# Kernel tuning notes

Hardware: AMD Instinct MI355X
Metric: run time of the kernel (lower is better)

The kernel has to match this reference:

```python
import jax, jax.numpy as jnp
import numpy as np

C = 128; D_STATE = 16; D_CONV = 4; EXPAND = 2
DI = EXPAND * C          # 256 inner dim
DT_RANK = (C + 15) // 16 # 8
NM, T, V = 32, 64, 22


def _mamba(x, in_w, conv_w, conv_b, xproj_w, dt_w, dt_b, Alog, Dp, out_w):
    """Standard Mamba block. x: (B, L, C) -> (B, L, C)."""
    B_, L, _ = x.shape
    xz = x @ in_w.T                       # (B, L, 2*DI)
    xi, z = jnp.split(xz, 2, axis=-1)     # each (B, L, DI)
    # causal depthwise conv over L, kernel D_CONV
    K = conv_w.shape[-1]
    xp = jnp.pad(xi, ((0, 0), (K - 1, 0), (0, 0)))
    xc = conv_b + sum(xp[:, k:k + L, :] * conv_w[:, k] for k in range(K))
    xc = jax.nn.silu(xc)
    dbl = xc @ xproj_w.T                  # (B, L, DT_RANK + 2*D_STATE)
    dt, Bm, Cm = jnp.split(dbl, [DT_RANK, DT_RANK + D_STATE], axis=-1)
    dt = jax.nn.softplus(dt @ dt_w.T + dt_b)   # (B, L, DI)
    A = -jnp.exp(Alog)                    # (DI, D_STATE), strictly negative

    def step(h, inp):
        dt_l, B_l, C_l, u_l = inp         # (B,DI) (B,DS) (B,DS) (B,DI)
        dA = jnp.exp(dt_l[:, :, None] * A)             # (B, DI, DS)
        h = dA * h + (dt_l * u_l)[:, :, None] * B_l[:, None, :]
        y = jnp.einsum('bds,bs->bd', h, C_l)
        return h, y

    h0 = jnp.zeros((B_, DI, D_STATE), x.dtype)
    xs = (jnp.moveaxis(dt, 1, 0), jnp.moveaxis(Bm, 1, 0),
          jnp.moveaxis(Cm, 1, 0), jnp.moveaxis(xc, 1, 0))
    _, ys = jax.lax.scan(step, h0, xs)    # ys: (L, B, DI)
    y = jnp.moveaxis(ys, 0, 1) + xc * Dp  # skip connection
    y = y * jax.nn.silu(z)
    return y @ out_w.T                    # (B, L, C)


def setup_inputs() -> dict:
    key = jax.random.key(0)
    ks = jax.random.split(key, 40)
    i = [0]
    def nrm(shape, s=0.05):
        i[0] += 1
        return jax.random.normal(ks[i[0]], shape, jnp.float32) * s
    inp = {"x": jax.random.normal(ks[0], (NM, C, T, V), jnp.float32)}
    for p in ("f", "b"):
        inp[p + "_in_w"] = nrm((2 * DI, C))
        inp[p + "_conv_w"] = nrm((DI, D_CONV), 0.2)
        inp[p + "_conv_b"] = nrm((DI,))
        inp[p + "_xproj_w"] = nrm((DT_RANK + 2 * D_STATE, DI))
        inp[p + "_dt_w"] = nrm((DI, DT_RANK), 0.1)
        inp[p + "_dt_b"] = nrm((DI,), 0.1)
        i[0] += 1
        inp[p + "_Alog"] = jax.random.uniform(ks[i[0]], (DI, D_STATE), jnp.float32)
        inp[p + "_D"] = nrm((DI,), 1.0)
        inp[p + "_out_w"] = nrm((C, DI))
    inp["fuse_w"] = nrm((C, 2 * C))
    inp["ln_w"] = jnp.ones((C,), jnp.float32)
    inp["ln_b"] = jnp.zeros((C,), jnp.float32)
    return inp


def reference(x, f_in_w, f_conv_w, f_conv_b, f_xproj_w, f_dt_w, f_dt_b, f_Alog, f_D, f_out_w,
              b_in_w, b_conv_w, b_conv_b, b_xproj_w, b_dt_w, b_dt_b, b_Alog, b_D, b_out_w,
              fuse_w, ln_w, ln_b):
    nm, c, t, v = x.shape
    xs = jnp.transpose(x, (0, 2, 3, 1)).reshape(nm * t, v, c)   # (B, V, C)
    fwd = _mamba(xs, f_in_w, f_conv_w, f_conv_b, f_xproj_w, f_dt_w, f_dt_b, f_Alog, f_D, f_out_w)
    bwd = _mamba(xs[:, ::-1, :], b_in_w, b_conv_w, b_conv_b, b_xproj_w, b_dt_w, b_dt_b, b_Alog, b_D, b_out_w)[:, ::-1, :]
    y = jnp.concatenate([fwd, bwd], axis=-1) @ fuse_w.T         # (B, V, C)
    mu = y.mean(-1, keepdims=True)
    var = y.var(-1, keepdims=True)
    y = (y - mu) / jnp.sqrt(var + 1e-5) * ln_w + ln_b
    return jnp.transpose(y.reshape(nm, t, v, c), (0, 3, 1, 2))  # (NM, C, T, V)
```

## Files before the change

kernel.cpp:

```cpp
#include <hip/hip_runtime.h>
#include <hip/hip_bf16.h>
#include <math.h>

namespace {

typedef unsigned short u16;
typedef unsigned int u32;

constexpr int LSEQ = 22, CD = 128, DI = 256, TDIM = 64;

constexpr int XS_LD = 136;
constexpr int XI_LD = 264;
constexpr int Y2_LD = 132;

constexpr int K1_XS = 0;
constexpr int K1_XI = 2992;
constexpr int K1_Z  = 8800;
constexpr int K1_N  = 14608;

constexpr int K2_N  = 11616;

constexpr int WS_F_IN_HI = 0;
constexpr int WS_F_IN_LO = 65536;
constexpr int WS_B_IN_HI = 131072;
constexpr int WS_B_IN_LO = 196608;
constexpr int WS_F_OUT   = 262144;
constexpr int WS_B_OUT   = 294912;
constexpr int WS_FUSE    = 327680;
constexpr int WS_F_XP_HI = 360448;
constexpr int WS_F_XP_LO = 372736;
constexpr int WS_B_XP_HI = 385024;
constexpr int WS_B_XP_LO = 397312;
constexpr int WS_TOTAL   = 409600;
constexpr int WS_Y       = 409600;

typedef __attribute__((ext_vector_type(8))) short bf16x8;
typedef __attribute__((ext_vector_type(4))) float f32x4;

__device__ __forceinline__ u16 f2bf(float f) {
  __bf16 b = (__bf16)f;
  return *reinterpret_cast<u16*>(&b);
}
__device__ __forceinline__ float bf2f(u16 h) {
  return __uint_as_float(((u32)h) << 16);
}
__device__ __forceinline__ float sigm(float x) {
  float e = __builtin_amdgcn_exp2f(-1.44269504f * x);
  return __builtin_amdgcn_rcpf(1.0f + e);
}

__global__ void prep_weights(const float* __restrict__ f_in, const float* __restrict__ b_in,
                             const float* __restrict__ f_xp, const float* __restrict__ b_xp,
                             u16* __restrict__ ws) {
  int i = blockIdx.x * 256 + threadIdx.x;
  if (i >= WS_TOTAL) return;
  u16 r = 0;
  if (i < WS_F_IN_LO) {
    r = f2bf(f_in[i]);
  } else if (i < WS_B_IN_HI) {
    float v = f_in[i - WS_F_IN_LO];
    r = f2bf(v - bf2f(f2bf(v)));
  } else if (i < WS_B_IN_LO) {
    r = f2bf(b_in[i - WS_B_IN_HI]);
  } else if (i < WS_F_OUT) {
    float v = b_in[i - WS_B_IN_LO];
    r = f2bf(v - bf2f(f2bf(v)));
  } else if (i < WS_F_XP_HI) {
    r = 0;
  } else if (i < WS_F_XP_LO) {
    int j = i - WS_F_XP_HI, n = j >> 8, k = j & 255;
    r = (n < 40) ? f2bf(f_xp[n * 256 + k]) : (u16)0;
  } else if (i < WS_B_XP_HI) {
    int j = i - WS_F_XP_LO, n = j >> 8, k = j & 255;
    if (n < 40) { float v = f_xp[n * 256 + k]; r = f2bf(v - bf2f(f2bf(v))); } else r = 0;
  } else if (i < WS_B_XP_LO) {
    int j = i - WS_B_XP_HI, n = j >> 8, k = j & 255;
    r = (n < 40) ? f2bf(b_xp[n * 256 + k]) : (u16)0;
  } else {
    int j = i - WS_B_XP_LO, n = j >> 8, k = j & 255;
    if (n < 40) { float v = b_xp[n * 256 + k]; r = f2bf(v - bf2f(f2bf(v))); } else r = 0;
  }
  ws[i] = r;
}

__global__ void prep_fold(const float* __restrict__ f_out, const float* __restrict__ b_out,
                          const float* __restrict__ fuse, u16* __restrict__ ws) {
  int i = blockIdx.x * 256 + threadIdx.x;
  int half = i >> 15;
  int j = i & 32767;
  int c = j >> 8, d = j & 255;
  const float* ow = half ? b_out : f_out;
  const float* fw = fuse + c * 256 + half * 128;
  float acc = 0.f;
#pragma unroll 4
  for (int k = 0; k < 128; ++k) acc = fmaf(fw[k], ow[k * 256 + d], acc);
  ws[(half ? WS_B_OUT : WS_F_OUT) + c * 256 + d] = f2bf(acc);
}

__global__ __launch_bounds__(256, 4) void mamba_scan_kernel(
    const float* __restrict__ x,
    const float* __restrict__ f_conv_w, const float* __restrict__ f_conv_b,
    const float* __restrict__ f_dt_w, const float* __restrict__ f_dt_b,
    const float* __restrict__ f_Alog, const float* __restrict__ f_D,
    const float* __restrict__ b_conv_w, const float* __restrict__ b_conv_b,
    const float* __restrict__ b_dt_w, const float* __restrict__ b_dt_b,
    const float* __restrict__ b_Alog, const float* __restrict__ b_D,
    u16* __restrict__ ws)
{
  __shared__ __align__(16) u16 pool[K1_N];

  u16* xs  = pool + K1_XS;
  u16* xiD = pool + K1_XI;
  u16* zD  = pool + K1_Z;

  const int tid = threadIdx.x;
  const int wv = tid >> 6, ln = tid & 63, lr = ln & 15, lg = ln >> 4;
  const int bid = blockIdx.x;
  const int b = bid >> 1, dir = bid & 1;
  const int nm = b / TDIM, t = b - nm * TDIM;
  const size_t base = (size_t)nm * CD * (TDIM * LSEQ) + (size_t)t * LSEQ;

  const int ra0 = (lr < LSEQ) ? lr : (LSEQ - 1);
  const int ra1 = (16 + lr < LSEQ) ? (16 + lr) : (LSEQ - 1);

#pragma unroll
  for (int k = 0; k < 11; ++k) {
    int idx = tid + k * 256;
    int c = idx / LSEQ, v = idx - c * LSEQ;
    xs[v * XS_LD + c] = f2bf(x[base + (size_t)c * (TDIM * LSEQ) + v]);
  }
  __syncthreads();

  {
    bf16x8 afr[2][4];
#pragma unroll
    for (int kt = 0; kt < 4; ++kt) {
      afr[0][kt] = *(const bf16x8*)&xs[ra0 * XS_LD + kt * 32 + lg * 8];
      afr[1][kt] = *(const bf16x8*)&xs[ra1 * XS_LD + kt * 32 + lg * 8];
    }
    const u16* ih = ws + (dir ? WS_B_IN_HI : WS_F_IN_HI);
    const u16* il = ws + (dir ? WS_B_IN_LO : WS_F_IN_LO);
    u16* dst = (wv < 2) ? xiD : zD;
    const bool isz = (wv >= 2);
    const int cb0 = (wv & 1) * 128;
#pragma unroll
    for (int half = 0; half < 2; ++half) {
      f32x4 acc[2][4];
#pragma unroll
      for (int m = 0; m < 2; ++m)
#pragma unroll
        for (int n = 0; n < 4; ++n) acc[m][n] = f32x4{0.f, 0.f, 0.f, 0.f};
#pragma unroll
      for (int kt = 0; kt < 4; ++kt) {
        bf16x8 bh[4], bl[4];
#pragma unroll
        for (int n = 0; n < 4; ++n) {
          const int off = (wv * 128 + (half * 4 + n) * 16 + lr) * 128 + kt * 32 + lg * 8;
          bh[n] = *(const bf16x8*)(ih + off);
          bl[n] = *(const bf16x8*)(il + off);
        }
#pragma unroll
        for (int n = 0; n < 4; ++n) {
          acc[0][n] = __builtin_amdgcn_mfma_f32_16x16x32_bf16(afr[0][kt], bh[n], acc[0][n], 0, 0, 0);
          acc[0][n] = __builtin_amdgcn_mfma_f32_16x16x32_bf16(afr[0][kt], bl[n], acc[0][n], 0, 0, 0);
          acc[1][n] = __builtin_amdgcn_mfma_f32_16x16x32_bf16(afr[1][kt], bh[n], acc[1][n], 0, 0, 0);
          acc[1][n] = __builtin_amdgcn_mfma_f32_16x16x32_bf16(afr[1][kt], bl[n], acc[1][n], 0, 0, 0);
        }
      }
#pragma unroll
      for (int m = 0; m < 2; ++m)
#pragma unroll
        for (int n = 0; n < 4; ++n)
#pragma unroll
          for (int j = 0; j < 4; ++j) {
            int row = 16 * m + lg * 4 + j;
            if (row < LSEQ) {
              int rr = dir ? (LSEQ - 1 - row) : row;
              float v = acc[m][n][j];
              if (isz) v = v * sigm(v);
              dst[rr * XI_LD + cb0 + half * 64 + n * 16 + lr] = f2bf(v);
            }
          }
    }
  }
  __syncthreads();

  {
    const int d = tid;
    const float* cw  = dir ? b_conv_w : f_conv_w;
    const float* cbp = dir ? b_conv_b : f_conv_b;
    float4 w4 = *(const float4*)(cw + d * 4);
    float bb = cbp[d];
    float w0 = 0.f, w1 = 0.f, w2 = 0.f;
    float nxt = bf2f(xiD[d]);
#pragma unroll
    for (int l = 0; l < LSEQ; ++l) {
      float w3 = nxt;
      if (l + 1 < LSEQ) nxt = bf2f(xiD[(l + 1) * XI_LD + d]);
      float a = fmaf(w0, w4.x, bb);
      a = fmaf(w1, w4.y, a);
      a = fmaf(w2, w4.z, a);
      a = fmaf(w3, w4.w, a);
      float s = a * sigm(a);
      xiD[l * XI_LD + d] = f2bf(s);
      w0 = w1; w1 = w2; w2 = w3;
    }
  }
  __syncthreads();

  for (int tt = wv; tt < 6; tt += 4) {
    const int mt = tt / 3, nt = tt - mt * 3;
    const u16* xph = ws + (dir ? WS_B_XP_HI : WS_F_XP_HI);
    const u16* xpl = ws + (dir ? WS_B_XP_LO : WS_F_XP_LO);
    const int raa = (mt * 16 + lr < LSEQ) ? (mt * 16 + lr) : (LSEQ - 1);
    f32x4 acc = f32x4{0.f, 0.f, 0.f, 0.f};
    const u16* bh_p = xph + (nt * 16 + lr) * 256 + lg * 8;
    const u16* bl_p = xpl + (nt * 16 + lr) * 256 + lg * 8;
#pragma unroll
    for (int kt = 0; kt < 8; kt += 2) {
      bf16x8 a0  = *(const bf16x8*)&xiD[raa * XI_LD + kt * 32 + lg * 8];
      bf16x8 a1  = *(const bf16x8*)&xiD[raa * XI_LD + (kt + 1) * 32 + lg * 8];
      bf16x8 bh0 = *(const bf16x8*)(bh_p + kt * 32);
      bf16x8 bl0 = *(const bf16x8*)(bl_p + kt * 32);
      bf16x8 bh1 = *(const bf16x8*)(bh_p + (kt + 1) * 32);
      bf16x8 bl1 = *(const bf16x8*)(bl_p + (kt + 1) * 32);
      acc = __builtin_amdgcn_mfma_f32_16x16x32_bf16(a0, bh0, acc, 0, 0, 0);
      acc = __builtin_amdgcn_mfma_f32_16x16x32_bf16(a0, bl0, acc, 0, 0, 0);
      acc = __builtin_amdgcn_mfma_f32_16x16x32_bf16(a1, bh1, acc, 0, 0, 0);
      acc = __builtin_amdgcn_mfma_f32_16x16x32_bf16(a1, bl1, acc, 0, 0, 0);
    }
    const int col = nt * 16 + lr;
    float* dtD = (float*)pool;
    float* bcD = ((float*)pool) + 176;
#pragma unroll
    for (int j = 0; j < 4; ++j) {
      int row = mt * 16 + lg * 4 + j;
      if (row < LSEQ) {
        if (col < 8) dtD[row * 8 + col] = acc[j];
        else if (col < 40) bcD[row * 32 + (col - 8)] = acc[j];
      }
    }
  }
  __syncthreads();

  {
    const int d = tid;
    const float* dtw  = dir ? b_dt_w : f_dt_w;
    const float* dtb  = dir ? b_dt_b : f_dt_b;
    const float* Alog = dir ? b_Alog : f_Alog;
    const float* Dp   = dir ? b_D : f_D;
    const float* dtD  = (const float*)pool;
    const float* bcD  = ((const float*)pool) + 176;
    const u16* gD  = zD;
    const u16* xcD = xiD;

    float4 dw0 = *(const float4*)(dtw + d * 8);
    float4 dw1 = *(const float4*)(dtw + d * 8 + 4);
    const float dtbv = dtb[d];
    float Av2[16];
#pragma unroll
    for (int s4 = 0; s4 < 4; ++s4) {
      float4 a = *(const float4*)(Alog + d * 16 + s4 * 4);
      Av2[s4 * 4 + 0] = -__expf(a.x) * 1.44269504f;
      Av2[s4 * 4 + 1] = -__expf(a.y) * 1.44269504f;
      Av2[s4 * 4 + 2] = -__expf(a.z) * 1.44269504f;
      Av2[s4 * 4 + 3] = -__expf(a.w) * 1.44269504f;
    }
    const float Dd = Dp[d];
    u16* wsY = ws + WS_Y + (size_t)b * 11264 + dir * 5632;
    const int r0 = dir ? (LSEQ - 1) : 0;
    const int rstep = dir ? -1 : 1;

    auto softp8 = [&](float4 q0, float4 q1) -> float {
      float sdt = dtbv;
      sdt = fmaf(q0.x, dw0.x, sdt); sdt = fmaf(q0.y, dw0.y, sdt);
      sdt = fmaf(q0.z, dw0.z, sdt); sdt = fmaf(q0.w, dw0.w, sdt);
      sdt = fmaf(q1.x, dw1.x, sdt); sdt = fmaf(q1.y, dw1.y, sdt);
      sdt = fmaf(q1.z, dw1.z, sdt); sdt = fmaf(q1.w, dw1.w, sdt);
      return (sdt > 20.f) ? sdt : __logf(1.f + __expf(sdt));
    };

    float h[16];
#pragma unroll
    for (int s = 0; s < 16; ++s) h[s] = 0.f;

#define SC(s, bv, cv) { float dA = __builtin_amdgcn_exp2f(dtv * Av2[s]); \
      h[s] = fmaf(dA, h[s], du * (bv)); \
      acc = fmaf(h[s], (cv), acc); }
    auto STEP = [&](int l, float dtv) {
      float u = bf2f(xcD[l * XI_LD + d]);
      float g = bf2f(gD[l * XI_LD + d]);
      float4 b0 = *(const float4*)(bcD + l * 32);
      float4 b1 = *(const float4*)(bcD + l * 32 + 4);
      float4 b2 = *(const float4*)(bcD + l * 32 + 8);
      float4 b3 = *(const float4*)(bcD + l * 32 + 12);
      float4 c0 = *(const float4*)(bcD + l * 32 + 16);
      float4 c1 = *(const float4*)(bcD + l * 32 + 20);
      float4 c2 = *(const float4*)(bcD + l * 32 + 24);
      float4 c3 = *(const float4*)(bcD + l * 32 + 28);
      float du = dtv * u;
      float acc = 0.f;
      SC(0, b0.x, c0.x) SC(1, b0.y, c0.y) SC(2, b0.z, c0.z) SC(3, b0.w, c0.w)
      SC(4, b1.x, c1.x) SC(5, b1.y, c1.y) SC(6, b1.z, c1.z) SC(7, b1.w, c1.w)
      SC(8, b2.x, c2.x) SC(9, b2.y, c2.y) SC(10, b2.z, c2.z) SC(11, b2.w, c2.w)
      SC(12, b3.x, c3.x) SC(13, b3.y, c3.y) SC(14, b3.z, c3.z) SC(15, b3.w, c3.w)
      float yo = fmaf(u, Dd, acc) * g;
      wsY[(r0 + rstep * l) * DI + d] = f2bf(yo);
    };
#undef SC

    float4 qa0 = *(const float4*)(dtD + 0);
    float4 qa1 = *(const float4*)(dtD + 4);
    float4 qb0 = *(const float4*)(dtD + 8);
    float4 qb1 = *(const float4*)(dtD + 12);
    float dtvA = softp8(qa0, qa1);
    float dtvB = softp8(qb0, qb1);

    for (int ll = 0; ll < LSEQ; ll += 2) {
      const int l2 = (ll + 2 < LSEQ) ? (ll + 2) : (LSEQ - 2);
      qa0 = *(const float4*)(dtD + l2 * 8);
      qa1 = *(const float4*)(dtD + l2 * 8 + 4);
      qb0 = *(const float4*)(dtD + l2 * 8 + 8);
      qb1 = *(const float4*)(dtD + l2 * 8 + 12);
      STEP(ll, dtvA);
      STEP(ll + 1, dtvB);
      dtvA = softp8(qa0, qa1);
      dtvB = softp8(qb0, qb1);
    }
  }
}

__global__ __launch_bounds__(256, 6) void fold_ln_kernel(
    const float* __restrict__ ln_w, const float* __restrict__ ln_b,
    const u16* __restrict__ ws, float* __restrict__ out)
{
  __shared__ __align__(16) u16 pool[K2_N];

  const int tid = threadIdx.x;
  const int wv = tid >> 6, ln = tid & 63, lr = ln & 15, lg = ln >> 4;
  const int b = blockIdx.x;
  const int nm = b / TDIM, t = b - nm * TDIM;
  const size_t base = (size_t)nm * CD * (TDIM * LSEQ) + (size_t)t * LSEQ;
  const u16* wsY = ws + WS_Y + (size_t)b * 11264;

  for (int idx = tid; idx < 2 * LSEQ * 32; idx += 256) {
    int dirc = idx / 704, r = idx - dirc * 704;
    int l = r >> 5, ch = (r & 31) * 8;
    *(bf16x8*)&pool[dirc * 5808 + l * XI_LD + ch] =
        *(const bf16x8*)(wsY + dirc * 5632 + l * 256 + ch);
  }
  __syncthreads();

  const int ra0 = (lr < LSEQ) ? lr : (LSEQ - 1);
  const int ra1 = (16 + lr < LSEQ) ? (16 + lr) : (LSEQ - 1);

  f32x4 acc[2][2];
#pragma unroll
  for (int m = 0; m < 2; ++m)
#pragma unroll
    for (int n = 0; n < 2; ++n) acc[m][n] = f32x4{0.f, 0.f, 0.f, 0.f};
#pragma unroll
  for (int dirc = 0; dirc < 2; ++dirc) {
    const u16* wp = ws + (dirc ? WS_B_OUT : WS_F_OUT);
    const u16* yD = pool + dirc * 5808;
#pragma unroll
    for (int kt = 0; kt < 8; ++kt) {
      bf16x8 a0 = *(const bf16x8*)&yD[ra0 * XI_LD + kt * 32 + lg * 8];
      bf16x8 a1 = *(const bf16x8*)&yD[ra1 * XI_LD + kt * 32 + lg * 8];
#pragma unroll
      for (int n = 0; n < 2; ++n) {
        bf16x8 bw = *(const bf16x8*)(wp + (wv * 32 + n * 16 + lr) * 256 + kt * 32 + lg * 8);
        acc[0][n] = __builtin_amdgcn_mfma_f32_16x16x32_bf16(a0, bw, acc[0][n], 0, 0, 0);
        acc[1][n] = __builtin_amdgcn_mfma_f32_16x16x32_bf16(a1, bw, acc[1][n], 0, 0, 0);
      }
    }
  }
  __syncthreads();

  float* y2 = (float*)pool;
#pragma unroll
  for (int m = 0; m < 2; ++m)
#pragma unroll
    for (int n = 0; n < 2; ++n)
#pragma unroll
      for (int j = 0; j < 4; ++j) {
        int row = 16 * m + lg * 4 + j;
        if (row < LSEQ) y2[row * Y2_LD + wv * 32 + n * 16 + lr] = acc[m][n][j];
      }
  __syncthreads();

  float* mu_s = (float*)(pool + 5808);
  float* rs_s = mu_s + LSEQ;
  for (int l = wv; l < LSEQ; l += 4) {
    float v1 = y2[l * Y2_LD + ln];
    float v2 = y2[l * Y2_LD + 64 + ln];
    float s = v1 + v2;
    float sq = v1 * v1 + v2 * v2;
#pragma unroll
    for (int m = 1; m < 64; m <<= 1) {
      s  += __shfl_xor(s, m, 64);
      sq += __shfl_xor(sq, m, 64);
    }
    if (ln == 0) {
      float mu = s * (1.0f / 128.0f);
      float var = sq * (1.0f / 128.0f) - mu * mu;
      mu_s[l] = mu;
      rs_s[l] = rsqrtf(var + 1e-5f);
    }
  }
  __syncthreads();

  for (int idx = tid; idx < LSEQ * CD; idx += 256) {
    int c = idx / LSEQ, v = idx - c * LSEQ;
    float yv = y2[v * Y2_LD + c];
    float o = (yv - mu_s[v]) * rs_s[v] * ln_w[c] + ln_b[c];
    out[base + (size_t)c * (TDIM * LSEQ) + v] = o;
  }
}

}

extern "C" void kernel_launch(void* const* d_in, const int* in_sizes, int n_in,
                              void* d_out, int out_size, void* d_ws, size_t ws_size,
                              hipStream_t stream) {
  (void)in_sizes; (void)n_in; (void)ws_size; (void)out_size;
  const float* p[22];
  for (int i = 0; i < 22; ++i) p[i] = (const float*)d_in[i];
  u16* ws = (u16*)d_ws;
  prep_weights<<<dim3((WS_TOTAL + 255) / 256), dim3(256), 0, stream>>>(
      p[1], p[10], p[4], p[13], ws);
  prep_fold<<<dim3(256), dim3(256), 0, stream>>>(p[9], p[18], p[19], ws);
  mamba_scan_kernel<<<dim3(32 * 64 * 2), dim3(256), 0, stream>>>(
      p[0],
      p[2], p[3], p[5], p[6], p[7], p[8],
      p[11], p[12], p[14], p[15], p[16], p[17],
      ws);
  fold_ln_kernel<<<dim3(32 * 64), dim3(256), 0, stream>>>(
      p[20], p[21], ws, (float*)d_out);
}
```

Baseline: 318.6 us.

## Shrink scan LDS by spilling gate to workspace and aliasing buffers

Reduces the scan kernel's shared memory footprint so more blocks fit per CU. The input tile buffer is reused for the xi buffer after a new barrier, dtD/bcD get dedicated regions, and when the workspace is large enough the silu(z) gate goes to global memory instead of LDS. Launch bounds rise to 8 (global-gate variant) or 6 (LDS variant) blocks per CU. In exchange it adds global write and read traffic for the gate, one extra barrier, and padding changes that may alter LDS bank conflicts.

Result: slower. 580.0 us (+82.0%).

```diff
diff --git a/kernel.cpp b/kernel.cpp
--- a/kernel.cpp
+++ b/kernel.cpp
@@ -9,14 +9,17 @@
 
 constexpr int LSEQ = 22, CD = 128, DI = 256, TDIM = 64;
 
-constexpr int XS_LD = 136;
-constexpr int XI_LD = 264;
+constexpr int XS_LD = 132;
+constexpr int XI_LD = 260;
 constexpr int Y2_LD = 132;
 
-constexpr int K1_XS = 0;
-constexpr int K1_XI = 2992;
-constexpr int K1_Z  = 8800;
-constexpr int K1_N  = 14608;
+constexpr int G_XI   = 0;
+constexpr int G_DTBC = 5720;
+constexpr int G_N    = 7480;
+constexpr int L_XI   = 0;
+constexpr int L_Z    = 5720;
+constexpr int L_DTBC = 11440;
+constexpr int L_N    = 13200;
 
 constexpr int K2_N  = 11616;
 
@@ -33,6 +36,8 @@
 constexpr int WS_B_XP_LO = 397312;
 constexpr int WS_TOTAL   = 409600;
 constexpr int WS_Y       = 409600;
+constexpr int WS_G       = WS_Y + 2048 * 11264;
+constexpr size_t WS_NEED_G = (size_t)(WS_G + 2048 * 11264) * 2;
 
 typedef __attribute__((ext_vector_type(8))) short bf16x8;
 typedef __attribute__((ext_vector_type(4))) float f32x4;
@@ -97,7 +102,9 @@
   ws[(half ? WS_B_OUT : WS_F_OUT) + c * 256 + d] = f2bf(acc);
 }
 
-__global__ __launch_bounds__(256, 4) void mamba_scan_kernel(
+template <bool ZWS>
+__device__ __forceinline__ void mamba_scan_body(
+    u16* pool,
     const float* __restrict__ x,
     const float* __restrict__ f_conv_w, const float* __restrict__ f_conv_b,
     const float* __restrict__ f_dt_w, const float* __restrict__ f_dt_b,
@@ -107,11 +114,11 @@
     const float* __restrict__ b_Alog, const float* __restrict__ b_D,
     u16* __restrict__ ws)
 {
-  __shared__ __align__(16) u16 pool[K1_N];
-
-  u16* xs  = pool + K1_XS;
-  u16* xiD = pool + K1_XI;
-  u16* zD  = pool + K1_Z;
+  u16* xs  = pool;
+  u16* xiD = pool + (ZWS ? G_XI : L_XI);
+  u16* zD  = ZWS ? nullptr : (pool + L_Z);
+  float* dtD = (float*)(pool + (ZWS ? G_DTBC : L_DTBC));
+  float* bcD = dtD + 176;
 
   const int tid = threadIdx.x;
   const int wv = tid >> 6, ln = tid & 63, lr = ln & 15, lg = ln >> 4;
@@ -119,6 +126,7 @@
   const int b = bid >> 1, dir = bid & 1;
   const int nm = b / TDIM, t = b - nm * TDIM;
   const size_t base = (size_t)nm * CD * (TDIM * LSEQ) + (size_t)t * LSEQ;
+  u16* wsG = ZWS ? (ws + WS_G + (size_t)b * 11264 + dir * 5632) : nullptr;
 
   const int ra0 = (lr < LSEQ) ? lr : (LSEQ - 1);
   const int ra1 = (16 + lr < LSEQ) ? (16 + lr) : (LSEQ - 1);
@@ -138,9 +146,10 @@
       afr[0][kt] = *(const bf16x8*)&xs[ra0 * XS_LD + kt * 32 + lg * 8];
       afr[1][kt] = *(const bf16x8*)&xs[ra1 * XS_LD + kt * 32 + lg * 8];
     }
+    __syncthreads();
+
     const u16* ih = ws + (dir ? WS_B_IN_HI : WS_F_IN_HI);
     const u16* il = ws + (dir ? WS_B_IN_LO : WS_F_IN_LO);
-    u16* dst = (wv < 2) ? xiD : zD;
     const bool isz = (wv >= 2);
     const int cb0 = (wv & 1) * 128;
 #pragma unroll
@@ -176,9 +185,15 @@
             int row = 16 * m + lg * 4 + j;
             if (row < LSEQ) {
               int rr = dir ? (LSEQ - 1 - row) : row;
+              int col = cb0 + half * 64 + n * 16 + lr;
               float v = acc[m][n][j];
-              if (isz) v = v * sigm(v);
-              dst[rr * XI_LD + cb0 + half * 64 + n * 16 + lr] = f2bf(v);
+              if (!isz) {
+                xiD[rr * XI_LD + col] = f2bf(v);
+              } else {
+                float g = v * sigm(v);
+                if (ZWS) wsG[rr * DI + col] = f2bf(g);
+                else     zD[rr * XI_LD + col] = f2bf(g);
+              }
             }
           }
     }
@@ -230,8 +245,6 @@
       acc = __builtin_amdgcn_mfma_f32_16x16x32_bf16(a1, bl1, acc, 0, 0, 0);
     }
     const int col = nt * 16 + lr;
-    float* dtD = (float*)pool;
-    float* bcD = ((float*)pool) + 176;
 #pragma unroll
     for (int j = 0; j < 4; ++j) {
       int row = mt * 16 + lg * 4 + j;
@@ -249,9 +262,6 @@
     const float* dtb  = dir ? b_dt_b : f_dt_b;
     const float* Alog = dir ? b_Alog : f_Alog;
     const float* Dp   = dir ? b_D : f_D;
-    const float* dtD  = (const float*)pool;
-    const float* bcD  = ((const float*)pool) + 176;
-    const u16* gD  = zD;
     const u16* xcD = xiD;
 
     float4 dw0 = *(const float4*)(dtw + d * 8);
@@ -289,7 +299,7 @@
       acc = fmaf(h[s], (cv), acc); }
     auto STEP = [&](int l, float dtv) {
       float u = bf2f(xcD[l * XI_LD + d]);
-      float g = bf2f(gD[l * XI_LD + d]);
+      float g = ZWS ? bf2f(wsG[l * DI + d]) : bf2f(zD[l * XI_LD + d]);
       float4 b0 = *(const float4*)(bcD + l * 32);
       float4 b1 = *(const float4*)(bcD + l * 32 + 4);
       float4 b2 = *(const float4*)(bcD + l * 32 + 8);
@@ -330,6 +340,28 @@
   }
 }
 
+#define SCAN_ARGS_DECL                                                        \
+    const float* __restrict__ x,                                              \
+    const float* __restrict__ f_conv_w, const float* __restrict__ f_conv_b,   \
+    const float* __restrict__ f_dt_w, const float* __restrict__ f_dt_b,       \
+    const float* __restrict__ f_Alog, const float* __restrict__ f_D,          \
+    const float* __restrict__ b_conv_w, const float* __restrict__ b_conv_b,   \
+    const float* __restrict__ b_dt_w, const float* __restrict__ b_dt_b,       \
+    const float* __restrict__ b_Alog, const float* __restrict__ b_D,          \
+    u16* __restrict__ ws
+#define SCAN_ARGS x, f_conv_w, f_conv_b, f_dt_w, f_dt_b, f_Alog, f_D,         \
+    b_conv_w, b_conv_b, b_dt_w, b_dt_b, b_Alog, b_D, ws
+
+__global__ __launch_bounds__(256, 8) void mamba_scan_g(SCAN_ARGS_DECL) {
+  __shared__ __align__(16) u16 pool[G_N];
+  mamba_scan_body<true>(pool, SCAN_ARGS);
+}
+
+__global__ __launch_bounds__(256, 6) void mamba_scan_l(SCAN_ARGS_DECL) {
+  __shared__ __align__(16) u16 pool[L_N];
+  mamba_scan_body<false>(pool, SCAN_ARGS);
+}
+
 __global__ __launch_bounds__(256, 6) void fold_ln_kernel(
     const float* __restrict__ ln_w, const float* __restrict__ ln_b,
     const u16* __restrict__ ws, float* __restrict__ out)
@@ -346,7 +378,7 @@
   for (int idx = tid; idx < 2 * LSEQ * 32; idx += 256) {
     int dirc = idx / 704, r = idx - dirc * 704;
     int l = r >> 5, ch = (r & 31) * 8;
-    *(bf16x8*)&pool[dirc * 5808 + l * XI_LD + ch] =
+    *(bf16x8*)&pool[dirc * 5808 + l * 264 + ch] =
         *(const bf16x8*)(wsY + dirc * 5632 + l * 256 + ch);
   }
   __syncthreads();
@@ -365,8 +397,8 @@
     const u16* yD = pool + dirc * 5808;
 #pragma unroll
     for (int kt = 0; kt < 8; ++kt) {
-      bf16x8 a0 = *(const bf16x8*)&yD[ra0 * XI_LD + kt * 32 + lg * 8];
-      bf16x8 a1 = *(const bf16x8*)&yD[ra1 * XI_LD + kt * 32 + lg * 8];
+      bf16x8 a0 = *(const bf16x8*)&yD[ra0 * 264 + kt * 32 + lg * 8];
+      bf16x8 a1 = *(const bf16x8*)&yD[ra1 * 264 + kt * 32 + lg * 8];
 #pragma unroll
       for (int n = 0; n < 2; ++n) {
         bf16x8 bw = *(const bf16x8*)(wp + (wv * 32 + n * 16 + lr) * 256 + kt * 32 + lg * 8);
@@ -423,18 +455,26 @@
 extern "C" void kernel_launch(void* const* d_in, const int* in_sizes, int n_in,
                               void* d_out, int out_size, void* d_ws, size_t ws_size,
                               hipStream_t stream) {
-  (void)in_sizes; (void)n_in; (void)ws_size; (void)out_size;
+  (void)in_sizes; (void)n_in; (void)out_size;
   const float* p[22];
   for (int i = 0; i < 22; ++i) p[i] = (const float*)d_in[i];
   u16* ws = (u16*)d_ws;
   prep_weights<<<dim3((WS_TOTAL + 255) / 256), dim3(256), 0, stream>>>(
       p[1], p[10], p[4], p[13], ws);
   prep_fold<<<dim3(256), dim3(256), 0, stream>>>(p[9], p[18], p[19], ws);
-  mamba_scan_kernel<<<dim3(32 * 64 * 2), dim3(256), 0, stream>>>(
-      p[0],
-      p[2], p[3], p[5], p[6], p[7], p[8],
-      p[11], p[12], p[14], p[15], p[16], p[17],
-      ws);
+  if (ws_size >= WS_NEED_G) {
+    mamba_scan_g<<<dim3(32 * 64 * 2), dim3(256), 0, stream>>>(
+        p[0],
+        p[2], p[3], p[5], p[6], p[7], p[8],
+        p[11], p[12], p[14], p[15], p[16], p[17],
+        ws);
+  } else {
+    mamba_scan_l<<<dim3(32 * 64 * 2), dim3(256), 0, stream>>>(
+        p[0],
+        p[2], p[3], p[5], p[6], p[7], p[8],
+        p[11], p[12], p[14], p[15], p[16], p[17],
+        ws);
+  }
   fold_ln_kernel<<<dim3(32 * 64), dim3(256), 0, stream>>>(
       p[20], p[21], ws, (float*)d_out);
 }
```

## Shrink scan kernel LDS by aliasing input tile and raise occupancy target

Applied to the files above, without the earlier changes.

Overlays the input x tile with the xi/z buffers, adding a barrier after the A fragments are loaded into registers, and gives dt/B/C their own region. Row strides shrink from 136/264 to 132/260 elements. Together these cut the scan kernel's shared memory so launch bounds can ask for 6 blocks per CU instead of 4, to hide latency in the serial scan. The costs are an extra barrier, tighter register limits that may spill, and new padding that can change LDS bank conflicts and 16-byte vector-load alignment.

New measurement: 392.6 us. 23.2% more time.

```diff
diff --git a/kernel.cpp b/kernel.cpp
--- a/kernel.cpp
+++ b/kernel.cpp
@@ -9,14 +9,14 @@
 
 constexpr int LSEQ = 22, CD = 128, DI = 256, TDIM = 64;
 
-constexpr int XS_LD = 136;
-constexpr int XI_LD = 264;
+constexpr int XS_LD = 132;
+constexpr int XI_LD = 260;
 constexpr int Y2_LD = 132;
 
-constexpr int K1_XS = 0;
-constexpr int K1_XI = 2992;
-constexpr int K1_Z  = 8800;
-constexpr int K1_N  = 14608;
+constexpr int L_XI   = 0;
+constexpr int L_Z    = 5720;
+constexpr int L_DTBC = 11440;
+constexpr int L_N    = 13200;
 
 constexpr int K2_N  = 11616;
 
@@ -97,7 +97,7 @@
   ws[(half ? WS_B_OUT : WS_F_OUT) + c * 256 + d] = f2bf(acc);
 }
 
-__global__ __launch_bounds__(256, 4) void mamba_scan_kernel(
+__global__ __launch_bounds__(256, 6) void mamba_scan_kernel(
     const float* __restrict__ x,
     const float* __restrict__ f_conv_w, const float* __restrict__ f_conv_b,
     const float* __restrict__ f_dt_w, const float* __restrict__ f_dt_b,
@@ -107,11 +107,13 @@
     const float* __restrict__ b_Alog, const float* __restrict__ b_D,
     u16* __restrict__ ws)
 {
-  __shared__ __align__(16) u16 pool[K1_N];
-
-  u16* xs  = pool + K1_XS;
-  u16* xiD = pool + K1_XI;
-  u16* zD  = pool + K1_Z;
+  __shared__ __align__(16) u16 pool[L_N];
+
+  u16* xs  = pool;
+  u16* xiD = pool + L_XI;
+  u16* zD  = pool + L_Z;
+  float* dtD = (float*)(pool + L_DTBC);
+  float* bcD = dtD + 176;
 
   const int tid = threadIdx.x;
   const int wv = tid >> 6, ln = tid & 63, lr = ln & 15, lg = ln >> 4;
@@ -138,6 +140,8 @@
       afr[0][kt] = *(const bf16x8*)&xs[ra0 * XS_LD + kt * 32 + lg * 8];
       afr[1][kt] = *(const bf16x8*)&xs[ra1 * XS_LD + kt * 32 + lg * 8];
     }
+    __syncthreads();
+
     const u16* ih = ws + (dir ? WS_B_IN_HI : WS_F_IN_HI);
     const u16* il = ws + (dir ? WS_B_IN_LO : WS_F_IN_LO);
     u16* dst = (wv < 2) ? xiD : zD;
@@ -176,9 +180,10 @@
             int row = 16 * m + lg * 4 + j;
             if (row < LSEQ) {
               int rr = dir ? (LSEQ - 1 - row) : row;
+              int col = cb0 + half * 64 + n * 16 + lr;
               float v = acc[m][n][j];
               if (isz) v = v * sigm(v);
-              dst[rr * XI_LD + cb0 + half * 64 + n * 16 + lr] = f2bf(v);
+              dst[rr * XI_LD + col] = f2bf(v);
             }
           }
     }
@@ -230,8 +235,6 @@
       acc = __builtin_amdgcn_mfma_f32_16x16x32_bf16(a1, bl1, acc, 0, 0, 0);
     }
     const int col = nt * 16 + lr;
-    float* dtD = (float*)pool;
-    float* bcD = ((float*)pool) + 176;
 #pragma unroll
     for (int j = 0; j < 4; ++j) {
       int row = mt * 16 + lg * 4 + j;
@@ -249,9 +252,6 @@
     const float* dtb  = dir ? b_dt_b : f_dt_b;
     const float* Alog = dir ? b_Alog : f_Alog;
     const float* Dp   = dir ? b_D : f_D;
-    const float* dtD  = (const float*)pool;
-    const float* bcD  = ((const float*)pool) + 176;
-    const u16* gD  = zD;
     const u16* xcD = xiD;
 
     float4 dw0 = *(const float4*)(dtw + d * 8);
@@ -289,7 +289,7 @@
       acc = fmaf(h[s], (cv), acc); }
     auto STEP = [&](int l, float dtv) {
       float u = bf2f(xcD[l * XI_LD + d]);
-      float g = bf2f(gD[l * XI_LD + d]);
+      float g = bf2f(zD[l * XI_LD + d]);
       float4 b0 = *(const float4*)(bcD + l * 32);
       float4 b1 = *(const float4*)(bcD + l * 32 + 4);
       float4 b2 = *(const float4*)(bcD + l * 32 + 8);
@@ -346,7 +346,7 @@
   for (int idx = tid; idx < 2 * LSEQ * 32; idx += 256) {
     int dirc = idx / 704, r = idx - dirc * 704;
     int l = r >> 5, ch = (r & 31) * 8;
-    *(bf16x8*)&pool[dirc * 5808 + l * XI_LD + ch] =
+    *(bf16x8*)&pool[dirc * 5808 + l * 264 + ch] =
         *(const bf16x8*)(wsY + dirc * 5632 + l * 256 + ch);
   }
   __syncthreads();
@@ -365,8 +365,8 @@
     const u16* yD = pool + dirc * 5808;
 #pragma unroll
     for (int kt = 0; kt < 8; ++kt) {
-      bf16x8 a0 = *(const bf16x8*)&yD[ra0 * XI_LD + kt * 32 + lg * 8];
-      bf16x8 a1 = *(const bf16x8*)&yD[ra1 * XI_LD + kt * 32 + lg * 8];
+      bf16x8 a0 = *(const bf16x8*)&yD[ra0 * 264 + kt * 32 + lg * 8];
+      bf16x8 a1 = *(const bf16x8*)&yD[ra1 * 264 + kt * 32 + lg * 8];
 #pragma unroll
       for (int n = 0; n < 2; ++n) {
         bf16x8 bw = *(const bf16x8*)(wp + (wv * 32 + n * 16 + lr) * 256 + kt * 32 + lg * 8);
```
